# Kernel tuning notes

Hardware: AMD Instinct MI355X
Metric: run time of the kernel (lower is better)

Reference implementation:

```python
import jax, jax.numpy as jnp
import numpy as np

N, IN, HID, OUT, C, H = 50000, 1488, 1024, 512, 32, 8
E = 800000

def setup_inputs() -> dict:
    key = jax.random.key(0)
    ks = jax.random.split(key, 16)
    s = lambda k, shape, fan: jax.random.normal(k, shape, jnp.float32) * (1.0 / np.sqrt(fan))
    return {
        "x": jax.random.normal(ks[0], (N, IN), jnp.float32),
        "edge_index": jax.random.randint(ks[1], (2, E), 0, N, jnp.int64),
        "ln_g": jnp.ones((IN,), jnp.float32),
        "ln_b": jnp.zeros((IN,), jnp.float32),
        "W1": s(ks[2], (IN, HID), IN), "b1": jnp.zeros((HID,), jnp.float32),
        "W2": s(ks[3], (HID, OUT), HID), "b2": jnp.zeros((OUT,), jnp.float32),
        "Wr": s(ks[4], (OUT, C * H), OUT), "br": jnp.zeros((C * H,), jnp.float32),
        "Wg": s(ks[5], (OUT, C * H), OUT),
        "att_src": s(ks[6], (H, C), C),
        "att_dst": s(ks[7], (H, C), C),
        "bg": jnp.zeros((C * H,), jnp.float32),
    }

def reference(x, edge_index, ln_g, ln_b, W1, b1, W2, b2, Wr, br, Wg, att_src, att_dst, bg):
    n = x.shape[0]
    # LayerNorm
    mu = jnp.mean(x, axis=-1, keepdims=True)
    var = jnp.mean(jnp.square(x - mu), axis=-1, keepdims=True)
    xn = (x - mu) * jax.lax.rsqrt(var + 1e-5) * ln_g + ln_b
    # init_proj MLP
    h = jax.nn.relu(xn @ W1 + b1) @ W2 + b2            # [N, OUT]
    res = h @ Wr + br                                   # [N, H*C]
    # GATConv (add_self_loops=True, dropout inactive in eval)
    loops = jnp.arange(n, dtype=edge_index.dtype)
    src = jnp.concatenate([edge_index[0], loops])
    dst = jnp.concatenate([edge_index[1], loops])
    g = (h @ Wg).reshape(n, H, C)                       # [N, H, C]
    a_src = jnp.sum(g * att_src, axis=-1)               # [N, H]
    a_dst = jnp.sum(g * att_dst, axis=-1)               # [N, H]
    e = jax.nn.leaky_relu(a_src[src] + a_dst[dst], 0.2) # [E', H]
    m = jax.ops.segment_max(e, dst, num_segments=n)     # per-dst softmax (stable)
    ex = jnp.exp(e - m[dst])
    denom = jax.ops.segment_sum(ex, dst, num_segments=n)
    alpha = ex / (denom[dst] + 1e-16)                   # [E', H]
    msg = alpha[:, :, None] * g[src]                    # [E', H, C]
    agg = jax.ops.segment_sum(msg, dst, num_segments=n) # [N, H, C]
    out = agg.reshape(n, H * C) + bg
    return jax.nn.elu(out) + res
```

## Files before the change

kernel.cpp:

```cpp
#include <hip/hip_runtime.h>
#include <hip/hip_bf16.h>
#include <cstdint>
#include <cstddef>

#define NND 50000
#define DIN 1488
#define DINP 1536
#define DHID 1024
#define DOUT 512
#define DHC 256
#define NE 800000
#define NHD 8
#define SPLITC 256

typedef __attribute__((ext_vector_type(8))) short short8;
typedef __attribute__((ext_vector_type(4))) short short4v;
typedef __attribute__((ext_vector_type(4))) float f32x4;
typedef __attribute__((ext_vector_type(4))) int int4v;
typedef unsigned short ushort_t;

__device__ __forceinline__ unsigned short f2bf(float f){
  union { float f; unsigned u; } v; v.f = f;
  unsigned r = v.u + 0x7fffu + ((v.u >> 16) & 1u);
  return (unsigned short)(r >> 16);
}
__device__ __forceinline__ float bf2f(unsigned short u){
  union { unsigned u; float f; } v; v.u = ((unsigned)u) << 16;
  return v.f;
}

__device__ __forceinline__ void async16(const void* g, void* l){
  __builtin_amdgcn_global_load_lds((__attribute__((address_space(1))) void*)g,
                                   (__attribute__((address_space(3))) void*)l, 16, 0, 0);
}

__device__ __forceinline__ void tc_tile(const float* __restrict__ W,
                                        ushort_t* __restrict__ WT,
                                        int K, int Nn, int Kp, int bx, int by){
  __shared__ float tile[32][33];
  const int tx = threadIdx.x & 31, ty = threadIdx.x >> 5;
  const int k0 = bx*32, n0 = by*32;
  for (int i = ty; i < 32; i += 8){
    int k = k0 + i, n = n0 + tx;
    tile[i][tx] = (k < K && n < Nn) ? W[(size_t)k*Nn + n] : 0.f;
  }
  __syncthreads();
  for (int i = ty; i < 32; i += 8){
    int n = n0 + i, k = k0 + tx;
    if (n < Nn && k < Kp) WT[(size_t)n*Kp + k] = f2bf(tile[tx][i]);
  }
}
__global__ __launch_bounds__(256) void prep_kernel(const float* W1, const float* Wr,
                                                   const float* Wg, const float* W2,
                                                   const float* b2, const float* br,
                                                   ushort_t* W1T, ushort_t* WrgT,
                                                   ushort_t* W2bf, float* b2rg,
                                                   int* cnt){
  int b = blockIdx.x;
  if (b < 1536){ tc_tile(W1, W1T, DIN, DHID, DINP, b % 48, b / 48); return; }
  b -= 1536;
  if (b < 128){ tc_tile(Wr, WrgT, DOUT, DHC, DOUT, b % 16, b / 16); return; }
  b -= 128;
  if (b < 128){ tc_tile(Wg, WrgT + 256*DOUT, DOUT, DHC, DOUT, b % 16, b / 16); return; }
  b -= 128;
  if (b < 256){
    const int idx = (b*256 + threadIdx.x)*8;
    f32x4 v0 = *(const f32x4*)(W2 + idx);
    f32x4 v1 = *(const f32x4*)(W2 + idx + 4);
    union { ushort_t u[8]; short8 s; } o;
    o.u[0]=f2bf(v0.x); o.u[1]=f2bf(v0.y); o.u[2]=f2bf(v0.z); o.u[3]=f2bf(v0.w);
    o.u[4]=f2bf(v1.x); o.u[5]=f2bf(v1.y); o.u[6]=f2bf(v1.z); o.u[7]=f2bf(v1.w);
    *(short8*)(W2bf + idx) = o.s;
    return;
  }
  b -= 256;
  if (b < 2){
    const int c = b*256 + threadIdx.x;
    float acc = 0.f;
    if (c < 256){
      for (int j = 0; j < DOUT; ++j) acc += b2[j]*Wr[(size_t)j*DHC + c];
      acc += br[c];
    } else {
      const int cc = c - 256;
      for (int j = 0; j < DOUT; ++j) acc += b2[j]*Wg[(size_t)j*DHC + cc];
    }
    b2rg[c] = acc;
    return;
  }
  b -= 2;
  { int i = b*256 + threadIdx.x; if (i < NND) cnt[i] = 0; }
}

#define LN_BLOCKS 12500
__global__ __launch_bounds__(256) void ln_count(const float* __restrict__ x,
                                                const float* __restrict__ gw,
                                                const float* __restrict__ bw,
                                                ushort_t* __restrict__ xn,
                                                const int* __restrict__ ei,
                                                int* __restrict__ cnt){
  const int bid = blockIdx.x;
  if (bid >= LN_BLOCKS){
    int e = (bid - LN_BLOCKS)*256 + threadIdx.x;
    if (e < NE) atomicAdd(&cnt[ei[NE + e]], 1);
    return;
  }
  const int wid = threadIdx.x >> 6, lane = threadIdx.x & 63;
  const int row = bid*4 + wid;
  if (row >= NND) return;
  const float* xr = x + (size_t)row * DIN;
  float s = 0.f, sq = 0.f;
  for (int i = lane*4; i < DIN; i += 256){
    f32x4 v = *(const f32x4*)(xr + i);
    s  += v.x + v.y + v.z + v.w;
    sq += v.x*v.x + v.y*v.y + v.z*v.z + v.w*v.w;
  }
  #pragma unroll
  for (int o = 32; o; o >>= 1){ s += __shfl_xor(s, o); sq += __shfl_xor(sq, o); }
  const float mu = s * (1.f/DIN);
  const float var = sq * (1.f/DIN) - mu*mu;
  const float rstd = rsqrtf(var + 1e-5f);
  ushort_t* xo = xn + (size_t)row * DINP;
  for (int i = lane*4; i < DIN; i += 256){
    f32x4 v = *(const f32x4*)(xr + i);
    f32x4 gg = *(const f32x4*)(gw + i);
    f32x4 bb = *(const f32x4*)(bw + i);
    union { ushort_t u[4]; unsigned long long q; } o;
    o.u[0] = f2bf((v.x-mu)*rstd*gg.x + bb.x);
    o.u[1] = f2bf((v.y-mu)*rstd*gg.y + bb.y);
    o.u[2] = f2bf((v.z-mu)*rstd*gg.z + bb.z);
    o.u[3] = f2bf((v.w-mu)*rstd*gg.w + bb.w);
    *(unsigned long long*)(xo + i) = o.q;
  }
  if (lane < (DINP - DIN)) xo[DIN + lane] = 0;
}

template<int ACT, int MODE, int CB, int SCAN>
__global__ __launch_bounds__(256, 2) void gemm128(const ushort_t* __restrict__ A,
                                                  const ushort_t* __restrict__ BT,
                                                  const float* __restrict__ bias,
                                                  void* __restrict__ out0,
                                                  void* __restrict__ out1,
                                                  int M, int Nn, int K,
                                                  const int* __restrict__ cnt,
                                                  int* __restrict__ offs,
                                                  int* __restrict__ cur){
  __shared__ __align__(16) ushort_t lds[2][2][128*64];
  const int t = threadIdx.x, wid = t >> 6, lane = t & 63;

  if (SCAN == 1 && blockIdx.x == 0){
    int* buf = (int*)&lds[0][0][0];
    const int chunk = (NND + 255) >> 8;
    const int s0 = t*chunk;
    const int s1 = (s0 + chunk < NND) ? s0 + chunk : NND;
    int s = 0;
    for (int i = s0; i < s1; i += 4){
      int4v v = *(const int4v*)(cnt + i);
      s += v.x + v.y + v.z + v.w + 4;
    }
    buf[t] = s; __syncthreads();
    for (int o = 1; o < 256; o <<= 1){
      int xv = (t >= o) ? buf[t-o] : 0;
      __syncthreads();
      buf[t] += xv;
      __syncthreads();
    }
    int run = buf[t] - s;
    for (int i = s0; i < s1; i += 4){
      int4v v = *(const int4v*)(cnt + i);
      int4v cu;
      cu.x = run; run += v.x + 1;
      cu.y = run; run += v.y + 1;
      cu.z = run; run += v.z + 1;
      cu.w = run; run += v.w + 1;
      *(int4v*)(cur + i)  = cu;
      *(int4v*)(offs + i) = cu;
    }
    if (t == 255) offs[NND] = run;
    return;
  }

  const int bid = blockIdx.x - SCAN, nwg = gridDim.x - SCAN;
  const int q = nwg >> 3, r = nwg & 7;
  const int xcd = bid & 7, slot = bid >> 3;
  const int lg = (xcd < r ? xcd*(q+1) : r*(q+1) + (xcd - r)*q) + slot;
  const int brow = (lg / CB) * 128, bcol = (lg % CB) * 128;

  const int l8  = t >> 3;
  const int cb  = (t & 7) << 4;
  const int scb = cb ^ ((l8 & 7) << 4);
  const ushort_t* pAr[4]; const ushort_t* pBr[4];
  #pragma unroll
  for (int rd = 0; rd < 4; ++rd){
    int ra = brow + rd*32 + l8; ra = ra < M ? ra : M-1;
    int rb = bcol + rd*32 + l8; rb = rb < Nn ? rb : Nn-1;
    pAr[rd] = A  + (size_t)ra*K + (scb >> 1);
    pBr[rd] = BT + (size_t)rb*K + (scb >> 1);
  }
  const int w8 = wid * 8;

#define STAGE1(buf, kt) do {                                           \
    const int _o = (kt) * 64;                                          \
    _Pragma("unroll")                                                  \
    for (int _rd = 0; _rd < 4; ++_rd){                                 \
      async16(pAr[_rd] + _o, &lds[buf][0][(_rd*32 + w8)*64]);          \
      async16(pBr[_rd] + _o, &lds[buf][1][(_rd*32 + w8)*64]);          \
    }                                                                  \
  } while(0)

  f32x4 acc[4][4];
  #pragma unroll
  for (int i=0;i<4;i++)
    #pragma unroll
    for (int j=0;j<4;j++) acc[i][j] = (f32x4){0.f,0.f,0.f,0.f};

  const int wr = (wid >> 1)*64, wc = (wid & 1)*64;
  const int fr = lane & 15;
  const int kb0 = (lane >> 4) << 4;
  const int sx  = (fr & 7) << 4;
  const int ko0 = ((kb0      ) ^ sx) >> 1;
  const int ko1 = ((kb0 | 64 ) ^ sx) >> 1;

  const int nk = K >> 6;
  STAGE1(0, 0);
  STAGE1(1, 1);
  for (int kt = 0; kt < nk; ++kt){
    const ushort_t* bA = lds[kt & 1][0];
    const ushort_t* bB = lds[kt & 1][1];
    if (kt + 1 < nk) asm volatile("s_waitcnt vmcnt(8)" ::: "memory");
    else             asm volatile("s_waitcnt vmcnt(0)" ::: "memory");
    __builtin_amdgcn_s_barrier();
    short8 af[4][2], bf_[4][2];
    #pragma unroll
    for (int m=0;m<4;m++){
      const int ra = (wr + m*16 + fr)*64;
      const int rb = (wc + m*16 + fr)*64;
      af[m][0]  = *(const short8*)&bA[ra + ko0];
      af[m][1]  = *(const short8*)&bA[ra + ko1];
      bf_[m][0] = *(const short8*)&bB[rb + ko0];
      bf_[m][1] = *(const short8*)&bB[rb + ko1];
    }
    asm volatile("s_waitcnt lgkmcnt(0)" ::: "memory");
    __builtin_amdgcn_sched_barrier(0);
    __builtin_amdgcn_s_barrier();
    if (kt + 2 < nk) STAGE1(kt & 1, kt + 2);
    __builtin_amdgcn_s_setprio(1);
    #pragma unroll
    for (int m=0;m<4;m++)
      #pragma unroll
      for (int n=0;n<4;n++){
        acc[m][n] = __builtin_amdgcn_mfma_f32_16x16x32_bf16(af[m][0], bf_[n][0], acc[m][n], 0, 0, 0);
        acc[m][n] = __builtin_amdgcn_mfma_f32_16x16x32_bf16(af[m][1], bf_[n][1], acc[m][n], 0, 0, 0);
      }
    __builtin_amdgcn_s_setprio(0);
  }
#undef STAGE1

  bool isf32;
  float* outF = nullptr; ushort_t* outB = nullptr; int ostride = 0, ocb = 0;
  if (MODE == 0){ isf32 = true;  outF = (float*)out0;    ostride = Nn; ocb = bcol; }
  else if (MODE == 1){ isf32 = false; outB = (ushort_t*)out0; ostride = Nn; ocb = bcol; }
  else {
    if (bcol < SPLITC){ isf32 = true;  outF = (float*)out0;    ostride = SPLITC;      ocb = bcol; }
    else              { isf32 = false; outB = (ushort_t*)out1; ostride = Nn - SPLITC; ocb = bcol - SPLITC; }
  }
  float bv[4];
  #pragma unroll
  for (int n=0;n<4;n++){
    const int col = wc + n*16 + (lane & 15);
    float b = 0.f;
    if (MODE == 2){ if (isf32 && bias) b = bias[bcol + col]; }
    else if (bias) b = bias[bcol + col];
    bv[n] = b;
  }
  float* sF = (float*)&lds[0][0][0];
  ushort_t* sB = (ushort_t*)&lds[0][0][0];
  const int trow = t >> 3, tc16 = (t & 7) * 16;
  #pragma unroll
  for (int c = 0; c < 4; ++c){
    __syncthreads();
    if ((wid >> 1) == (c >> 1)){
      #pragma unroll
      for (int mm = 0; mm < 2; ++mm){
        const int m = 2*(c & 1) + mm;
        const int rbase = m*16 + (lane >> 4)*4 - (c & 1)*32;
        #pragma unroll
        for (int n = 0; n < 4; ++n){
          const int col = wc + n*16 + (lane & 15);
          #pragma unroll
          for (int j = 0; j < 4; ++j){
            float v = acc[m][n][j] + bv[n];
            if (ACT) v = v > 0.f ? v : 0.f;
            if (isf32) sF[(rbase + j)*128 + col] = v;
            else       sB[(rbase + j)*128 + col] = f2bf(v);
          }
        }
      }
    }
    __syncthreads();
    const int grow = brow + c*32 + trow;
    if (grow < M){
      if (isf32){
        float* dst = outF + (size_t)grow*ostride + ocb + tc16;
        const float* src = sF + trow*128 + tc16;
        #pragma unroll
        for (int q2 = 0; q2 < 4; ++q2) ((f32x4*)dst)[q2] = ((const f32x4*)src)[q2];
      } else {
        ushort_t* dst = outB + (size_t)grow*ostride + ocb + tc16;
        const ushort_t* src = sB + trow*128 + tc16;
        #pragma unroll
        for (int q2 = 0; q2 < 2; ++q2) ((short8*)dst)[q2] = ((const short8*)src)[q2];
      }
    }
  }
}

#define G2_NWG 392
template<int ACT, int MODE, int CB, int EXTRA>
__global__ __launch_bounds__(512, 2) void gemm256(const ushort_t* __restrict__ A,
                                                  const ushort_t* __restrict__ BT,
                                                  const float* __restrict__ bias,
                                                  void* __restrict__ out0,
                                                  void* __restrict__ out1,
                                                  int M, int Nn, int K,
                                                  const int* __restrict__ ei,
                                                  int* __restrict__ cur,
                                                  int* __restrict__ eidx,
                                                  const float* __restrict__ att_s,
                                                  const float* __restrict__ att_d,
                                                  float* __restrict__ asrc,
                                                  float* __restrict__ adst){
  __shared__ __align__(16) ushort_t lds[2][2][256*64];
  const int t = threadIdx.x, wid = t >> 6, lane = t & 63;

  if (EXTRA == 1 && blockIdx.x >= G2_NWG){
    int i = (blockIdx.x - G2_NWG)*512 + t;
    if (i < NND){
      int p = atomicAdd(&cur[i], 1); eidx[p] = i;
    } else if (i < NND + NE){
      int e = i - NND;
      int src = ei[e], dst = ei[NE + e];
      int p = atomicAdd(&cur[dst], 1);
      eidx[p] = src;
    }
    return;
  }

  const int bid = blockIdx.x, nwg = G2_NWG;
  const int q = nwg >> 3, r = nwg & 7;
  const int xcd = bid & 7, slot = bid >> 3;
  const int lg = (xcd < r ? xcd*(q+1) : r*(q+1) + (xcd - r)*q) + slot;
  const int brow = (lg / CB) * 256, bcol = (lg % CB) * 256;

  const int l8  = t >> 3;
  const int cb  = (t & 7) << 4;
  const unsigned scb = (unsigned)(cb ^ ((l8 & 7) << 4));
  unsigned rowA[4], rowB[4];
  #pragma unroll
  for (int rd = 0; rd < 4; ++rd){
    int ra = brow + rd*64 + l8; ra = ra < M ? ra : M-1;
    int rb = bcol + rd*64 + l8; rb = rb < Nn ? rb : Nn-1;
    rowA[rd] = (unsigned)ra * (unsigned)(K*2);
    rowB[rd] = (unsigned)rb * (unsigned)(K*2);
  }
  const int wst = (wid * 8) * 64;

#define STAGE2(buf, kt) do {                                              \
    const unsigned _ob = (unsigned)(kt)*128u + scb;                       \
    _Pragma("unroll")                                                     \
    for (int _rd = 0; _rd < 4; ++_rd){                                    \
      async16((const char*)A  + rowA[_rd] + _ob, &lds[buf][0][_rd*64*64 + wst]); \
      async16((const char*)BT + rowB[_rd] + _ob, &lds[buf][1][_rd*64*64 + wst]); \
    }                                                                     \
  } while(0)

  f32x4 acc[8][4];
  #pragma unroll
  for (int i=0;i<8;i++)
    #pragma unroll
    for (int j=0;j<4;j++) acc[i][j] = (f32x4){0.f,0.f,0.f,0.f};

  const int wrow = (wid >> 2), wcol = (wid & 3);
  const int fr = lane & 15;
  const int kb0 = (lane >> 4) << 4;
  const int sx  = (fr & 7) << 4;
  const int ko0 = ((kb0      ) ^ sx) >> 1;
  const int ko1 = ((kb0 | 64 ) ^ sx) >> 1;

  const int nk = K >> 6;
  STAGE2(0, 0);
  STAGE2(1, 1);
  for (int kt = 0; kt < nk; ++kt){
    const ushort_t* bA = lds[kt & 1][0];
    const ushort_t* bB = lds[kt & 1][1];
    if (kt + 1 < nk) asm volatile("s_waitcnt vmcnt(8)" ::: "memory");
    else             asm volatile("s_waitcnt vmcnt(0)" ::: "memory");
    __builtin_amdgcn_s_barrier();
    short8 af[8][2], bf_[4][2];
    #pragma unroll
    for (int m=0;m<8;m++){
      const int ra = (wrow*128 + m*16 + fr)*64;
      af[m][0] = *(const short8*)&bA[ra + ko0];
      af[m][1] = *(const short8*)&bA[ra + ko1];
    }
    #pragma unroll
    for (int n=0;n<4;n++){
      const int rb = (wcol*64 + n*16 + fr)*64;
      bf_[n][0] = *(const short8*)&bB[rb + ko0];
      bf_[n][1] = *(const short8*)&bB[rb + ko1];
    }
    asm volatile("s_waitcnt lgkmcnt(0)" ::: "memory");
    __builtin_amdgcn_sched_barrier(0);
    __builtin_amdgcn_s_barrier();
    if (kt + 2 < nk) STAGE2(kt & 1, kt + 2);
    __builtin_amdgcn_s_setprio(1);
    #pragma unroll
    for (int m=0;m<8;m++)
      #pragma unroll
      for (int n=0;n<4;n++){
        acc[m][n] = __builtin_amdgcn_mfma_f32_16x16x32_bf16(af[m][0], bf_[n][0], acc[m][n], 0, 0, 0);
        acc[m][n] = __builtin_amdgcn_mfma_f32_16x16x32_bf16(af[m][1], bf_[n][1], acc[m][n], 0, 0, 0);
      }
    __builtin_amdgcn_s_setprio(0);
  }
#undef STAGE2

  const bool isf32 = (MODE == 0) || (MODE == 2 && bcol == 0);
  float bv[4];
  #pragma unroll
  for (int n=0;n<4;n++){
    const int col = bcol + wcol*64 + n*16 + (lane & 15);
    float b = 0.f;
    if (MODE == 1){ if (bias) b = bias[col]; }
    if (MODE == 2){ b = bias[col]; }
    bv[n] = b;
  }

  if (isf32){
    float* outF; int ostride, ocb;
    if (MODE == 0){ outF = (float*)out0; ostride = Nn;  ocb = bcol; }
    else          { outF = (float*)out0; ostride = 256; ocb = 0;    }
    float* sF = (float*)&lds[0][0][0];
    #pragma unroll
    for (int p = 0; p < 2; ++p){
      __syncthreads();
      if (wrow == p){
        #pragma unroll
        for (int m=0;m<8;m++){
          const int row = m*16 + (lane >> 4)*4;
          #pragma unroll
          for (int n=0;n<4;n++){
            const int col = wcol*64 + n*16 + (lane & 15);
            #pragma unroll
            for (int j=0;j<4;j++){
              float v = acc[m][n][j] + bv[n];
              if (ACT) v = v > 0.f ? v : 0.f;
              sF[(row+j)*256 + col] = v;
            }
          }
        }
      }
      __syncthreads();
      const int srow = t >> 6, scol4 = (t & 63) * 4;
      #pragma unroll
      for (int rr = 0; rr < 16; ++rr){
        const int rloc = rr*8 + srow;
        const int grow = brow + p*128 + rloc;
        if (grow < M)
          *(f32x4*)(outF + (size_t)grow*ostride + ocb + scol4) = *(const f32x4*)&sF[rloc*256 + scol4];
      }
    }
  } else {
    ushort_t* outB; int ostride, ocb;
    if (MODE == 1){ outB = (ushort_t*)out0; ostride = Nn;  ocb = bcol; }
    else          { outB = (ushort_t*)out1; ostride = 256; ocb = 0;    }
    ushort_t* sB = (ushort_t*)&lds[0][0][0];
    __syncthreads();
    #pragma unroll
    for (int m=0;m<8;m++){
      const int row = wrow*128 + m*16 + (lane >> 4)*4;
      #pragma unroll
      for (int n=0;n<4;n++){
        const int col = wcol*64 + n*16 + (lane & 15);
        #pragma unroll
        for (int j=0;j<4;j++){
          float v = acc[m][n][j] + bv[n];
          if (ACT) v = v > 0.f ? v : 0.f;
          sB[(row+j)*256 + col] = f2bf(v);
        }
      }
    }
    __syncthreads();
    const int srow = t >> 5, scol8 = (t & 31) * 8;
    #pragma unroll
    for (int rr = 0; rr < 16; ++rr){
      const int rloc = rr*16 + srow;
      const int grow = brow + rloc;
      if (grow < M)
        *(short8*)(outB + (size_t)grow*ostride + ocb + scol8) = *(const short8*)&sB[rloc*256 + scol8];
    }
    if (MODE == 2){
      const int h = t & 7;
      const int hc0 = h * 32;
      #pragma unroll
      for (int k = 0; k < 4; ++k){
        const int rloc = (t >> 3) + k*64;
        const int grow = brow + rloc;
        if (grow < M){
          float a = 0.f, d = 0.f;
          #pragma unroll
          for (int c0 = 0; c0 < 32; c0 += 8){
            short8 gv = *(const short8*)&sB[rloc*256 + hc0 + c0];
            #pragma unroll
            for (int j = 0; j < 8; ++j){
              float g = bf2f((ushort_t)gv[j]);
              a += g*att_s[hc0 + c0 + j];
              d += g*att_d[hc0 + c0 + j];
            }
          }
          asrc[grow*NHD + h] = a;
          adst[grow*NHD + h] = d;
        }
      }
    }
  }
}

__global__ __launch_bounds__(256) void gat_agg(const int* __restrict__ offs,
                                               const int* __restrict__ eidx,
                                               const float* __restrict__ asrc,
                                               const float* __restrict__ adst,
                                               const ushort_t* __restrict__ gm,
                                               const float* __restrict__ res,
                                               const float* __restrict__ bg,
                                               float* __restrict__ out){
  const int wid = threadIdx.x >> 6, lane = threadIdx.x & 63;
  const int node = blockIdx.x*4 + wid;
  if (node >= NND) return;
  const int h = lane >> 3, jj = lane & 7;
  const int e0 = offs[node], deg = offs[node+1] - e0;
  const float adv = adst[node*NHD + h];

  float mx = -1e30f;
  for (int j = jj; j < deg; j += 8){
    int s = eidx[e0 + j];
    float e = asrc[s*NHD + h] + adv; e = e > 0.f ? e : 0.2f*e;
    mx = fmaxf(mx, e);
  }
  mx = fmaxf(mx, __shfl_xor(mx, 1));
  mx = fmaxf(mx, __shfl_xor(mx, 2));
  mx = fmaxf(mx, __shfl_xor(mx, 4));

  const int c4 = lane*4;
  float sm = 0.f;
  f32x4 acc = {0.f,0.f,0.f,0.f};
  for (int j0 = 0; j0 < deg; j0 += 8){
    const int cnt = (deg - j0) < 8 ? (deg - j0) : 8;
    int s = 0; float w = 0.f;
    if (jj < cnt){
      s = eidx[e0 + j0 + jj];
      float e = asrc[s*NHD + h] + adv; e = e > 0.f ? e : 0.2f*e;
      w = __expf(e - mx);
      sm += w;
    }
    #pragma unroll
    for (int u = 0; u < 8; ++u){
      if (u < cnt){
        const int   su = __builtin_amdgcn_readlane(s, u);
        const float wu = __shfl(w, (h << 3) | u);
        short4v gv = *(const short4v*)(gm + (size_t)su*DHC + c4);
        acc.x += wu*bf2f((ushort_t)gv.x);
        acc.y += wu*bf2f((ushort_t)gv.y);
        acc.z += wu*bf2f((ushort_t)gv.z);
        acc.w += wu*bf2f((ushort_t)gv.w);
      }
    }
  }
  sm += __shfl_xor(sm, 1); sm += __shfl_xor(sm, 2); sm += __shfl_xor(sm, 4);
  const float inv = 1.f/(sm + 1e-16f);

  f32x4 bgv = *(const f32x4*)(bg + c4);
  f32x4 rv  = *(const f32x4*)(res + (size_t)node*DHC + c4);
  f32x4 o;
  #pragma unroll
  for (int q = 0; q < 4; ++q){
    float v = acc[q]*inv + bgv[q];
    v = v > 0.f ? v : expm1f(v);
    o[q] = v + rv[q];
  }
  *(f32x4*)(out + (size_t)node*DHC + c4) = o;
}

extern "C" void kernel_launch(void* const* d_in, const int* in_sizes, int n_in,
                              void* d_out, int out_size, void* d_ws, size_t ws_size,
                              hipStream_t stream){
  (void)in_sizes; (void)n_in; (void)out_size; (void)ws_size;
  const float* x     = (const float*)d_in[0];
  const int*   ei    = (const int*)d_in[1];
  const float* ln_g  = (const float*)d_in[2];
  const float* ln_b  = (const float*)d_in[3];
  const float* W1    = (const float*)d_in[4];
  const float* b1    = (const float*)d_in[5];
  const float* W2    = (const float*)d_in[6];
  const float* b2    = (const float*)d_in[7];
  const float* Wr    = (const float*)d_in[8];
  const float* br    = (const float*)d_in[9];
  const float* Wg    = (const float*)d_in[10];
  const float* att_s = (const float*)d_in[11];
  const float* att_d = (const float*)d_in[12];
  const float* bg    = (const float*)d_in[13];
  float* out = (float*)d_out;

  char* p = (char*)d_ws;
  ushort_t* xn   = (ushort_t*)(p);
  ushort_t* h1   = (ushort_t*)(p + 153600000);
  float*    asrc = (float*)(p + 256000000);
  float*    adst = (float*)(p + 257600000);
  int*      cnt  = (int*)(p + 259200000);
  int*      offs = (int*)(p + 259400064);
  int*      cur  = (int*)(p + 259600128);
  int*      eidx = (int*)(p + 259800192);
  ushort_t* W1T  = (ushort_t*)d_out;
  ushort_t* WrgT = (ushort_t*)((char*)d_out + 3145728);
  ushort_t* W2bf = (ushort_t*)((char*)d_out + 3670016);
  ushort_t* WcT  = (ushort_t*)((char*)d_out + 4718592);
  float*    b2rg = (float*)((char*)d_out + 5767168);
  float*    res  = (float*)(p + 0);
  ushort_t* gm   = (ushort_t*)(p + 51200000);

  prep_kernel<<<2246, 256, 0, stream>>>(W1, Wr, Wg, W2, b2, br,
                                        W1T, WrgT, W2bf, b2rg, cnt);

  gemm128<0,1,8,0><<<32, 256, 0, stream>>>(WrgT, W2bf, nullptr, WcT, nullptr,
                                           512, 1024, 512, nullptr, nullptr, nullptr);

  ln_count<<<LN_BLOCKS + (NE + 255)/256, 256, 0, stream>>>(x, ln_g, ln_b, xn, ei, cnt);

  gemm128<1,1,8,1><<<3128 + 1, 256, 0, stream>>>(xn, W1T, b1, h1, nullptr,
                                                 NND, DHID, DINP, cnt, offs, cur);

  gemm256<0,2,2,1><<<G2_NWG + (NND + NE + 511)/512, 512, 0, stream>>>(
      h1, WcT, b2rg, res, gm, NND, 2*DHC, DHID,
      ei, cur, eidx, att_s, att_d, asrc, adst);

  gat_agg<<<(NND + 3)/4, 256, 0, stream>>>(offs, eidx, asrc, adst, gm, res, bg, out);
}
```

Before: 551.4 us.

## Replace first GEMM with 256x256-tile 8-wave kernel using phased pipelining

```diff
diff --git a/kernel.cpp b/kernel.cpp
--- a/kernel.cpp
+++ b/kernel.cpp
@@ -147,38 +147,6 @@
   __shared__ __align__(16) ushort_t lds[2][2][128*64];
   const int t = threadIdx.x, wid = t >> 6, lane = t & 63;
 
-  if (SCAN == 1 && blockIdx.x == 0){
-    int* buf = (int*)&lds[0][0][0];
-    const int chunk = (NND + 255) >> 8;
-    const int s0 = t*chunk;
-    const int s1 = (s0 + chunk < NND) ? s0 + chunk : NND;
-    int s = 0;
-    for (int i = s0; i < s1; i += 4){
-      int4v v = *(const int4v*)(cnt + i);
-      s += v.x + v.y + v.z + v.w + 4;
-    }
-    buf[t] = s; __syncthreads();
-    for (int o = 1; o < 256; o <<= 1){
-      int xv = (t >= o) ? buf[t-o] : 0;
-      __syncthreads();
-      buf[t] += xv;
-      __syncthreads();
-    }
-    int run = buf[t] - s;
-    for (int i = s0; i < s1; i += 4){
-      int4v v = *(const int4v*)(cnt + i);
-      int4v cu;
-      cu.x = run; run += v.x + 1;
-      cu.y = run; run += v.y + 1;
-      cu.z = run; run += v.z + 1;
-      cu.w = run; run += v.w + 1;
-      *(int4v*)(cur + i)  = cu;
-      *(int4v*)(offs + i) = cu;
-    }
-    if (t == 255) offs[NND] = run;
-    return;
-  }
-
   const int bid = blockIdx.x - SCAN, nwg = gridDim.x - SCAN;
   const int q = nwg >> 3, r = nwg & 7;
   const int xcd = bid & 7, slot = bid >> 3;
@@ -311,6 +279,200 @@
         for (int q2 = 0; q2 < 2; ++q2) ((short8*)dst)[q2] = ((const short8*)src)[q2];
       }
     }
+  }
+}
+
+template<int ACT, int CB>
+__global__ __launch_bounds__(512, 1) void gemm256p8(const ushort_t* __restrict__ A,
+                                                    const ushort_t* __restrict__ BT,
+                                                    const float* __restrict__ bias,
+                                                    ushort_t* __restrict__ out0,
+                                                    int M, int Nn, int K,
+                                                    const int* __restrict__ cnt,
+                                                    int* __restrict__ offs,
+                                                    int* __restrict__ cur){
+  __shared__ __align__(16) ushort_t lds[2][2][2][64*128];
+  const int t = threadIdx.x, wid = t >> 6, lane = t & 63;
+
+  if (blockIdx.x == 0){
+    int* sbuf = (int*)&lds[0][0][0][0];
+    const int chunk = (NND + 255) >> 8;
+    int s = 0;
+    if (t < 256){
+      const int s0 = t*chunk;
+      const int s1 = (s0 + chunk < NND) ? s0 + chunk : NND;
+      for (int i = s0; i < s1; i += 4){
+        int4v v = *(const int4v*)(cnt + i);
+        s += v.x + v.y + v.z + v.w + 4;
+      }
+    }
+    sbuf[t] = s; __syncthreads();
+    for (int o = 1; o < 256; o <<= 1){
+      int xv = (t >= o && t < 256) ? sbuf[t-o] : 0;
+      __syncthreads();
+      if (t < 256) sbuf[t] += xv;
+      __syncthreads();
+    }
+    if (t < 256){
+      int run = sbuf[t] - s;
+      const int s0 = t*chunk;
+      const int s1 = (s0 + chunk < NND) ? s0 + chunk : NND;
+      for (int i = s0; i < s1; i += 4){
+        int4v v = *(const int4v*)(cnt + i);
+        int4v cu;
+        cu.x = run; run += v.x + 1;
+        cu.y = run; run += v.y + 1;
+        cu.z = run; run += v.z + 1;
+        cu.w = run; run += v.w + 1;
+        *(int4v*)(cur + i)  = cu;
+        *(int4v*)(offs + i) = cu;
+      }
+      if (t == 255) offs[NND] = run;
+    }
+    return;
+  }
+
+  const int bid = blockIdx.x - 1, nwg = gridDim.x - 1;
+  const int q = nwg >> 3, r = nwg & 7;
+  const int xcd = bid & 7, slot = bid >> 3;
+  const int lg = (xcd < r ? xcd*(q+1) : r*(q+1) + (xcd - r)*q) + slot;
+  const int brow = (lg / CB) * 256, bcol = (lg % CB) * 256;
+
+  const int l8  = t >> 3;
+  const int cb  = (t & 7) << 4;
+  const unsigned scb = (unsigned)(cb ^ ((l8 & 7) << 4));
+  unsigned rowA[2][2], rowB[2][2];
+  #pragma unroll
+  for (int hf = 0; hf < 2; ++hf)
+    #pragma unroll
+    for (int rd = 0; rd < 2; ++rd){
+      int ra = brow + hf*128 + rd*64 + l8; ra = ra < M ? ra : M-1;
+      int rb = bcol + hf*128 + rd*64 + l8; rb = rb < Nn ? rb : Nn-1;
+      rowA[hf][rd] = (unsigned)ra * (unsigned)(K*2);
+      rowB[hf][rd] = (unsigned)rb * (unsigned)(K*2);
+    }
+  const int w8 = wid * 8;
+
+#define STG_A(buf, hf, kt) do {                                               \
+    const unsigned _ob = (unsigned)(kt)*128u + scb;                           \
+    async16((const char*)A + rowA[hf][0] + _ob, &lds[buf][0][hf][(w8)*64]);   \
+    async16((const char*)A + rowA[hf][1] + _ob, &lds[buf][0][hf][(64+w8)*64]);\
+  } while(0)
+#define STG_B(buf, hf, kt) do {                                               \
+    const unsigned _ob = (unsigned)(kt)*128u + scb;                           \
+    async16((const char*)BT + rowB[hf][0] + _ob, &lds[buf][1][hf][(w8)*64]);  \
+    async16((const char*)BT + rowB[hf][1] + _ob, &lds[buf][1][hf][(64+w8)*64]);\
+  } while(0)
+
+  f32x4 acc[8][4];
+  #pragma unroll
+  for (int i=0;i<8;i++)
+    #pragma unroll
+    for (int j=0;j<4;j++) acc[i][j] = (f32x4){0.f,0.f,0.f,0.f};
+
+  const int wrow = (wid >> 2), wcol = (wid & 3);
+  const int fr = lane & 15;
+  const int kb0 = (lane >> 4) << 4;
+  const int sx  = (fr & 7) << 4;
+  const int ko0 = ((kb0      ) ^ sx) >> 1;
+  const int ko1 = ((kb0 | 64 ) ^ sx) >> 1;
+  const int bhalf = wcol >> 1, brl = (wcol & 1)*64;
+
+#define RD_A(buf, m) do {                                          \
+    const int _ra = ((m)*16 + fr)*64;                              \
+    af[m][0] = *(const short8*)&lds[buf][0][wrow][_ra + ko0];      \
+    af[m][1] = *(const short8*)&lds[buf][0][wrow][_ra + ko1];      \
+  } while(0)
+#define RD_B(buf, n) do {                                          \
+    const int _rb = (brl + (n)*16 + fr)*64;                        \
+    bf[n][0] = *(const short8*)&lds[buf][1][bhalf][_rb + ko0];     \
+    bf[n][1] = *(const short8*)&lds[buf][1][bhalf][_rb + ko1];     \
+  } while(0)
+#define SYNC_PH() do {                                             \
+    __builtin_amdgcn_s_barrier();                                  \
+    asm volatile("s_waitcnt lgkmcnt(0)" ::: "memory");             \
+    __builtin_amdgcn_sched_barrier(0);                             \
+  } while(0)
+#define MFMA_Q(M0, N0) do {                                        \
+    __builtin_amdgcn_s_setprio(1);                                 \
+    _Pragma("unroll")                                              \
+    for (int _m=(M0); _m<(M0)+4; ++_m)                             \
+      _Pragma("unroll")                                            \
+      for (int _n=(N0); _n<(N0)+2; ++_n){                          \
+        acc[_m][_n] = __builtin_amdgcn_mfma_f32_16x16x32_bf16(af[_m][0], bf[_n][0], acc[_m][_n], 0, 0, 0); \
+        acc[_m][_n] = __builtin_amdgcn_mfma_f32_16x16x32_bf16(af[_m][1], bf[_n][1], acc[_m][_n], 0, 0, 0); \
+      }                                                            \
+    __builtin_amdgcn_s_setprio(0);                                 \
+  } while(0)
+
+  const int nk = K >> 6;
+  STG_A(0,0,0); STG_A(0,1,0); STG_B(0,0,0); STG_B(0,1,0);
+  STG_A(1,0,1); STG_A(1,1,1);
+  asm volatile("s_waitcnt vmcnt(4)" ::: "memory");
+  __builtin_amdgcn_s_barrier();
+
+  for (int kt = 0; kt < nk; ++kt){
+    const int buf = kt & 1, obuf = buf ^ 1;
+    short8 af[8][2], bf[4][2];
+    RD_A(buf,0); RD_A(buf,1); RD_A(buf,2); RD_A(buf,3);
+    RD_B(buf,0); RD_B(buf,1);
+    if (kt + 1 < nk) STG_B(obuf, 0, kt + 1);
+    SYNC_PH();
+    MFMA_Q(0, 0);
+    RD_A(buf,4); RD_A(buf,5); RD_A(buf,6); RD_A(buf,7);
+    if (kt + 1 < nk) STG_B(obuf, 1, kt + 1);
+    SYNC_PH();
+    MFMA_Q(4, 0);
+    RD_B(buf,2); RD_B(buf,3);
+    if (kt + 2 < nk) STG_A(buf, 0, kt + 2);
+    SYNC_PH();
+    MFMA_Q(0, 2);
+    if (kt + 2 < nk){
+      STG_A(buf, 1, kt + 2);
+      asm volatile("s_waitcnt vmcnt(4)" ::: "memory");
+    } else {
+      asm volatile("s_waitcnt vmcnt(0)" ::: "memory");
+    }
+    __builtin_amdgcn_s_barrier();
+    MFMA_Q(4, 2);
+  }
+#undef STG_A
+#undef STG_B
+#undef RD_A
+#undef RD_B
+#undef SYNC_PH
+#undef MFMA_Q
+
+  float bv[4];
+  #pragma unroll
+  for (int n=0;n<4;n++){
+    const int col = bcol + wcol*64 + n*16 + (lane & 15);
+    bv[n] = bias ? bias[col] : 0.f;
+  }
+  ushort_t* sB = (ushort_t*)&lds[0][0][0][0];
+  __syncthreads();
+  #pragma unroll
+  for (int m=0;m<8;m++){
+    const int row = wrow*128 + m*16 + (lane >> 4)*4;
+    #pragma unroll
+    for (int n=0;n<4;n++){
+      const int col = wcol*64 + n*16 + (lane & 15);
+      #pragma unroll
+      for (int j=0;j<4;j++){
+        float v = acc[m][n][j] + bv[n];
+        if (ACT) v = v > 0.f ? v : 0.f;
+        sB[(row+j)*256 + col] = f2bf(v);
+      }
+    }
+  }
+  __syncthreads();
+  const int srow = t >> 5, scol8 = (t & 31) * 8;
+  #pragma unroll
+  for (int rr = 0; rr < 16; ++rr){
+    const int rloc = rr*16 + srow;
+    const int grow = brow + rloc;
+    if (grow < M)
+      *(short8*)(out0 + (size_t)grow*Nn + bcol + scol8) = *(const short8*)&sB[rloc*256 + scol8];
   }
 }
 
@@ -635,8 +797,8 @@
 
   ln_count<<<LN_BLOCKS + (NE + 255)/256, 256, 0, stream>>>(x, ln_g, ln_b, xn, ei, cnt);
 
-  gemm128<1,1,8,1><<<3128 + 1, 256, 0, stream>>>(xn, W1T, b1, h1, nullptr,
-                                                 NND, DHID, DINP, cnt, offs, cur);
+  gemm256p8<1,4><<<785, 512, 0, stream>>>(xn, W1T, b1, h1,
+                                          NND, DHID, DINP, cnt, offs, cur);
 
   gemm256<0,2,2,1><<<G2_NWG + (NND + NE + 511)/512, 512, 0, stream>>>(
       h1, WcT, b2rg, res, gm, NND, 2*DHC, DHID,
```

Result: faster. 530.4 us (-3.8%).
